# Kernel tuning notes

Measured on AMD Instinct MI355X. Metric: run time of the kernel, lower is better.

Reference implementation:

```python
import jax, jax.numpy as jnp
import numpy as np

EPS = 1e-6
S = 0.025
ALPHA = 0.98
DELTA = 2.0
R = 0.5


def setup_inputs() -> dict:
    key = jax.random.key(0)
    x = jax.random.uniform(key, (64, 128, 4000), dtype=jnp.float32)  # [B, n_mels, T]
    return {"x": x}


def reference(x):
    # PCEN: IIR (EMA) smoother over time + pow-based per-bin nonlinearity.
    # x: [B, M, T]
    delta_r = DELTA ** R

    def step(m_t, x_t):
        # m_t, x_t: [B, M]
        m_t = (1.0 - S) * m_t + S * x_t
        pcen = (x_t / (EPS + m_t) ** ALPHA + DELTA) ** R - delta_r
        return m_t, pcen

    xt = jnp.moveaxis(x, 2, 0)  # [T, B, M] for scan over time
    m0 = jnp.zeros(x.shape[:2], dtype=x.dtype)
    _, out = jax.lax.scan(step, m0, xt)  # out: [T, B, M]
    return jnp.moveaxis(out, 0, 2)  # [B, M, T]
```

## Files before the change

kernel.cpp:

```cpp
#include <hip/hip_runtime.h>


#define TT     4000
#define NROWS  8192
#define NFULL  15
#define TAILL  40

__global__ __launch_bounds__(256, 8) void pcen_kernel(const float* __restrict__ x,
                                                      float* __restrict__ out) {
    const int wid  = (blockIdx.x * blockDim.x + threadIdx.x) >> 6;
    const int lane = threadIdx.x & 63;

    const float S = 0.025f, A = 0.975f, EPS = 1e-6f, NA = -0.98f;
    const float SQRT2 = 1.41421356237f;

    const float A4   = A * A * A * A;
    const float A8   = A4 * A4;
    const float A16  = A8 * A8;
    const float A32  = A16 * A16;
    const float A64  = A32 * A32;
    const float A128 = A64 * A64;
    const float A256 = A128 * A128;

    float powAl = 1.0f;
    if (lane & 1)  powAl *= A4;
    if (lane & 2)  powAl *= A8;
    if (lane & 4)  powAl *= A16;
    if (lane & 8)  powAl *= A32;
    if (lane & 16) powAl *= A64;
    if (lane & 32) powAl *= A128;

    const float4* xi = (const float4*)(x   + (long)wid * TT) + lane;
    float4*       oi = (float4*)      (out + (long)wid * TT) + lane;

    float carry = 0.0f;

    #pragma unroll 2
    for (int it = 0; it <= NFULL; ++it) {
        const bool active = (it < NFULL) | (lane < TAILL);
        float4 v = make_float4(0.0f, 0.0f, 0.0f, 0.0f);
        if (active) v = xi[it * 64];

        float b = S * v.x;
        b = fmaf(A, b, S * v.y);
        b = fmaf(A, b, S * v.z);
        float B = fmaf(A, b, S * v.w);

        float t;
        t = __shfl_up(B, 1, 64);  B = fmaf(A4,   (lane >= 1)  ? t : 0.0f, B);
        t = __shfl_up(B, 2, 64);  B = fmaf(A8,   (lane >= 2)  ? t : 0.0f, B);
        t = __shfl_up(B, 4, 64);  B = fmaf(A16,  (lane >= 4)  ? t : 0.0f, B);
        t = __shfl_up(B, 8, 64);  B = fmaf(A32,  (lane >= 8)  ? t : 0.0f, B);
        t = __shfl_up(B, 16, 64); B = fmaf(A64,  (lane >= 16) ? t : 0.0f, B);
        t = __shfl_up(B, 32, 64); B = fmaf(A128, (lane >= 32) ? t : 0.0f, B);

        float bp = __shfl_up(B, 1, 64);
        float mprev = fmaf(powAl, carry, (lane >= 1) ? bp : 0.0f);

        float b63 = __shfl(B, 63, 64);
        carry = fmaf(A256, carry, b63);

        float m = mprev;
        float4 o;
        m = fmaf(A, m, S * v.x);
        o.x = sqrtf(fmaf(v.x, exp2f(NA * log2f(m + EPS)), 2.0f)) - SQRT2;
        m = fmaf(A, m, S * v.y);
        o.y = sqrtf(fmaf(v.y, exp2f(NA * log2f(m + EPS)), 2.0f)) - SQRT2;
        m = fmaf(A, m, S * v.z);
        o.z = sqrtf(fmaf(v.z, exp2f(NA * log2f(m + EPS)), 2.0f)) - SQRT2;
        m = fmaf(A, m, S * v.w);
        o.w = sqrtf(fmaf(v.w, exp2f(NA * log2f(m + EPS)), 2.0f)) - SQRT2;

        if (active) oi[it * 64] = o;
    }
}

extern "C" void kernel_launch(void* const* d_in, const int* in_sizes, int n_in,
                              void* d_out, int out_size, void* d_ws, size_t ws_size,
                              hipStream_t stream) {
    const float* x = (const float*)d_in[0];
    float* out = (float*)d_out;
    const int block = 256;
    const int grid = (NROWS * 64) / block;
    pcen_kernel<<<grid, block, 0, stream>>>(x, out);
}
```

Measured before the change: 48.61 us.

## Replace shuffle-based wave scan with DPP ops and hardware transcendental builtins

The log-step prefix scan across the wavefront now uses DPP row shifts and row broadcasts instead of LDS-permute shuffles. The exclusive prefix is recovered algebraically from the inclusive one rather than with an extra shuffle, and the carry uses readlane. The S factor is pulled out of the recurrence, and log/exp/sqrt use raw hardware builtins. This cuts cross-lane latency and instruction count, at the cost of some precision from the subtraction-based prefix and the unguarded transcendentals.

Result: no change. 48.36 us (-0.5%).

```diff
diff --git a/kernel.cpp b/kernel.cpp
--- a/kernel.cpp
+++ b/kernel.cpp
@@ -5,6 +5,9 @@
 #define NROWS  8192
 #define NFULL  15
 #define TAILL  40
+
+#define DPPF(x, ctrl, rmask) \
+    __int_as_float(__builtin_amdgcn_update_dpp(0, __float_as_int(x), (ctrl), (rmask), 0xf, false))
 
 __global__ __launch_bounds__(256, 8) void pcen_kernel(const float* __restrict__ x,
                                                       float* __restrict__ out) {
@@ -14,13 +17,15 @@
     const float S = 0.025f, A = 0.975f, EPS = 1e-6f, NA = -0.98f;
     const float SQRT2 = 1.41421356237f;
 
-    const float A4   = A * A * A * A;
+    const float A2   = A * A;
+    const float A4   = A2 * A2;
     const float A8   = A4 * A4;
     const float A16  = A8 * A8;
     const float A32  = A16 * A16;
     const float A64  = A32 * A32;
     const float A128 = A64 * A64;
     const float A256 = A128 * A128;
+    const float INVA4 = 1.0f / A4;
 
     float powAl = 1.0f;
     if (lane & 1)  powAl *= A4;
@@ -30,6 +35,14 @@
     if (lane & 16) powAl *= A64;
     if (lane & 32) powAl *= A128;
 
+    float p15 = 1.0f;
+    if (lane & 1) p15 *= A4;
+    if (lane & 2) p15 *= A8;
+    if (lane & 4) p15 *= A16;
+    if (lane & 8) p15 *= A32;
+    float w15 = A4 * p15;
+    float w31 = (lane & 16) ? (w15 * A64) : w15;
+
     const float4* xi = (const float4*)(x   + (long)wid * TT) + lane;
     float4*       oi = (float4*)      (out + (long)wid * TT) + lane;
 
@@ -38,38 +51,38 @@
     #pragma unroll 2
     for (int it = 0; it <= NFULL; ++it) {
         const bool active = (it < NFULL) | (lane < TAILL);
-        float4 v = make_float4(0.0f, 0.0f, 0.0f, 0.0f);
+        float4 v = make_float4(0.f, 0.f, 0.f, 0.f);
         if (active) v = xi[it * 64];
 
-        float b = S * v.x;
-        b = fmaf(A, b, S * v.y);
-        b = fmaf(A, b, S * v.z);
-        float B = fmaf(A, b, S * v.w);
+        float b = v.x;
+        b = fmaf(A, b, v.y);
+        b = fmaf(A, b, v.z);
+        float B0 = fmaf(A, b, v.w);
+        float B = B0;
 
-        float t;
-        t = __shfl_up(B, 1, 64);  B = fmaf(A4,   (lane >= 1)  ? t : 0.0f, B);
-        t = __shfl_up(B, 2, 64);  B = fmaf(A8,   (lane >= 2)  ? t : 0.0f, B);
-        t = __shfl_up(B, 4, 64);  B = fmaf(A16,  (lane >= 4)  ? t : 0.0f, B);
-        t = __shfl_up(B, 8, 64);  B = fmaf(A32,  (lane >= 8)  ? t : 0.0f, B);
-        t = __shfl_up(B, 16, 64); B = fmaf(A64,  (lane >= 16) ? t : 0.0f, B);
-        t = __shfl_up(B, 32, 64); B = fmaf(A128, (lane >= 32) ? t : 0.0f, B);
+        B = fmaf(A4,  DPPF(B, 0x111, 0xf), B);
+        B = fmaf(A8,  DPPF(B, 0x112, 0xf), B);
+        B = fmaf(A16, DPPF(B, 0x114, 0xf), B);
+        B = fmaf(A32, DPPF(B, 0x118, 0xf), B);
+        B = fmaf(w15, DPPF(B, 0x142, 0xa), B);
+        B = fmaf(w31, DPPF(B, 0x143, 0xc), B);
 
-        float bp = __shfl_up(B, 1, 64);
-        float mprev = fmaf(powAl, carry, (lane >= 1) ? bp : 0.0f);
+        float bp = (B - B0) * INVA4;
 
-        float b63 = __shfl(B, 63, 64);
+        float n = fmaf(powAl, carry, bp);
+
+        float b63 = __int_as_float(__builtin_amdgcn_readlane(__float_as_int(B), 63));
         carry = fmaf(A256, carry, b63);
 
-        float m = mprev;
         float4 o;
-        m = fmaf(A, m, S * v.x);
-        o.x = sqrtf(fmaf(v.x, exp2f(NA * log2f(m + EPS)), 2.0f)) - SQRT2;
-        m = fmaf(A, m, S * v.y);
-        o.y = sqrtf(fmaf(v.y, exp2f(NA * log2f(m + EPS)), 2.0f)) - SQRT2;
-        m = fmaf(A, m, S * v.z);
-        o.z = sqrtf(fmaf(v.z, exp2f(NA * log2f(m + EPS)), 2.0f)) - SQRT2;
-        m = fmaf(A, m, S * v.w);
-        o.w = sqrtf(fmaf(v.w, exp2f(NA * log2f(m + EPS)), 2.0f)) - SQRT2;
+        n = fmaf(A, n, v.x);
+        o.x = __builtin_amdgcn_sqrtf(fmaf(v.x, __builtin_amdgcn_exp2f(NA * __builtin_amdgcn_logf(fmaf(S, n, EPS))), 2.0f)) - SQRT2;
+        n = fmaf(A, n, v.y);
+        o.y = __builtin_amdgcn_sqrtf(fmaf(v.y, __builtin_amdgcn_exp2f(NA * __builtin_amdgcn_logf(fmaf(S, n, EPS))), 2.0f)) - SQRT2;
+        n = fmaf(A, n, v.z);
+        o.z = __builtin_amdgcn_sqrtf(fmaf(v.z, __builtin_amdgcn_exp2f(NA * __builtin_amdgcn_logf(fmaf(S, n, EPS))), 2.0f)) - SQRT2;
+        n = fmaf(A, n, v.w);
+        o.w = __builtin_amdgcn_sqrtf(fmaf(v.w, __builtin_amdgcn_exp2f(NA * __builtin_amdgcn_logf(fmaf(S, n, EPS))), 2.0f)) - SQRT2;
 
         if (active) oi[it * 64] = o;
     }
```
